# Kernel optimization log

Measured on AMD Instinct MI355X. Metric: run time of the kernel, lower is better.

The kernel has to match this reference:

```python
import jax, jax.numpy as jnp
import numpy as np

B = 1 << 20
N_FREQS = 6          # sin+cos -> 3*2*6 = 36 dims for position
N_BINS = 4           # one-blob bins -> 4 dims per scalar
W_SCALE = 0.18       # ~ sqrt(2/64) He init for ReLU


def freq_embed(p):
    # p: [B,3] -> [B, 3*2*N_FREQS] NeRF-style sin/cos frequency encoding
    freqs = (2.0 ** jnp.arange(N_FREQS, dtype=p.dtype)) * jnp.pi  # [F]
    ang = p[:, :, None] * freqs  # [B,3,F]
    return jnp.concatenate([jnp.sin(ang), jnp.cos(ang)], axis=-1).reshape(p.shape[0], -1)


def one_blob_embed(x):
    # x: [B,D] values in [0,1] -> [B, D*N_BINS] Gaussian one-blob encoding
    centers = (jnp.arange(N_BINS, dtype=x.dtype) + 0.5) / N_BINS  # [K]
    sigma = 1.0 / N_BINS
    val = jnp.exp(-0.5 * ((x[:, :, None] - centers) / sigma) ** 2)  # [B,D,K]
    return val.reshape(x.shape[0], -1)


def to_sphe_coords(d):
    # unit direction [B,3] -> normalized (theta, phi) in [0,1]^2
    theta = jnp.arccos(jnp.clip(d[:, 2], -1.0, 1.0)) / jnp.pi
    phi = jnp.arctan2(d[:, 1], d[:, 0]) / (2.0 * jnp.pi) + 0.5
    return jnp.stack([theta, phi], axis=-1)


def setup_inputs() -> dict:
    key = jax.random.key(0)
    ks = jax.random.split(key, 13)
    p = jax.random.normal(ks[0], (B, 3), dtype=jnp.float32)
    wi = jax.random.normal(ks[1], (B, 3), dtype=jnp.float32)
    wi = wi / jnp.linalg.norm(wi, axis=-1, keepdims=True)
    n = jax.random.normal(ks[2], (B, 3), dtype=jnp.float32)
    n = n / jnp.linalg.norm(n, axis=-1, keepdims=True)
    alpha = jax.random.uniform(ks[3], (B, 3), dtype=jnp.float32)
    beta = jax.random.uniform(ks[4], (B, 3), dtype=jnp.float32)
    r = jax.random.uniform(ks[5], (B, 1), dtype=jnp.float32)
    Ws = {}
    for i in range(6):
        Ws[f"W{i}"] = jax.random.normal(ks[6 + i], (64, 64), dtype=jnp.float32) * W_SCALE
    Ws["W6"] = jax.random.normal(ks[12], (3, 64), dtype=jnp.float32) * W_SCALE
    return dict(p=p, wi=wi, n=n, alpha=alpha, beta=beta, r=r, **Ws)


def reference(p, wi, n, alpha, beta, r, W0, W1, W2, W3, W4, W5, W6):
    x = jnp.concatenate([
        freq_embed(p),                               # 36
        one_blob_embed(to_sphe_coords(wi)),          # 8
        one_blob_embed(to_sphe_coords(n)),           # 8
        one_blob_embed(1.0 - jnp.exp(-r)),           # 4
        alpha,                                       # 3
        beta,                                        # 3
        jnp.ones_like(p[:, :2]),                     # 2 (implicit bias)
    ], axis=-1)  # [B,64]
    h = x
    for W in (W0, W1, W2, W3, W4, W5):
        h = jax.nn.relu(h @ W.T)
    out = h @ W6.T  # [B,3]
    return out * (alpha + beta)  # reflectance factorization
```

## Files before the change

kernel.cpp:

```cpp
#include <hip/hip_runtime.h>

typedef __attribute__((ext_vector_type(8))) short short8;
typedef __attribute__((ext_vector_type(4))) float f32x4;

typedef __attribute__((address_space(3))) unsigned short lds_us;
typedef const __attribute__((address_space(1))) unsigned short glb_us;

__device__ __forceinline__ unsigned short f2bf(float x) {
  union { float f; unsigned u; } v; v.f = x;
  unsigned r = v.u + 0x7fffu + ((v.u >> 16) & 1u);
  return (unsigned short)(r >> 16);
}

#if __has_builtin(__builtin_amdgcn_cvt_pk_bf16_f32)
__device__ __forceinline__ unsigned pk2(float a, float b) {
  return __builtin_bit_cast(unsigned, __builtin_amdgcn_cvt_pk_bf16_f32(a, b));
}
#else
__device__ __forceinline__ unsigned pk2(float a, float b) {
  union { float f; unsigned u; } x, y; x.f = a; y.f = b;
  return __builtin_amdgcn_perm(y.u + 0x8000u, x.u + 0x8000u, 0x07060302u);
}
#endif

__device__ __forceinline__ short8 u2s8(uint4 u) {
  union { uint4 a; short8 b; } c; c.a = u; return c.b;
}

__device__ __forceinline__ void wave_mem_fence() {
  asm volatile("" ::: "memory");
  __builtin_amdgcn_wave_barrier();
  asm volatile("" ::: "memory");
}

__device__ __forceinline__ void gload16(const unsigned short* g, unsigned short* l) {
  __builtin_amdgcn_global_load_lds((glb_us*)g, (lds_us*)l, 16, 0, 0);
}

__device__ __forceinline__ float acos01(float z) {
  float ax = fminf(fabsf(z), 1.0f);
  float t  = __builtin_amdgcn_sqrtf(1.0f - ax);
  float p  = fmaf(ax, fmaf(ax, fmaf(ax, -0.00596110f, 0.02363618f),
                           -0.06751692f), 0.49998766f);
  p *= t;
  return z >= 0.0f ? p : 1.0f - p;
}

__device__ __forceinline__ float atan2_01(float y, float x) {
  float ax = fabsf(x), ay = fabsf(y);
  float hi = fmaxf(ax, ay), lo = fminf(ax, ay);
  float r  = lo * __builtin_amdgcn_rcpf(fmaxf(hi, 1e-30f));
  float r2 = r * r;
  float p  = fmaf(r2, fmaf(r2, fmaf(r2, fmaf(r2, fmaf(r2,
               -0.0018655370f, 0.0083800422f), -0.018531250f),
                0.030803547f), -0.052940457f), 0.159151323f);
  float q  = r * p;
  q = (ay > ax) ? 0.25f - q : q;
  q = (x < 0.0f) ? 0.5f - q : q;
  return 0.5f + ((y >= 0.0f) ? q : -q);
}

__device__ __forceinline__ uint2 blob4pk(float x) {
  float x4 = x * 4.0f;
  float e0, e1, e2, e3;
  { float t = x4 - 0.5f; e0 = __builtin_amdgcn_exp2f(t * t * -0.72134752f); }
  { float t = x4 - 1.5f; e1 = __builtin_amdgcn_exp2f(t * t * -0.72134752f); }
  { float t = x4 - 2.5f; e2 = __builtin_amdgcn_exp2f(t * t * -0.72134752f); }
  { float t = x4 - 3.5f; e3 = __builtin_amdgcn_exp2f(t * t * -0.72134752f); }
  return make_uint2(pk2(e0, e1), pk2(e2, e3));
}

__global__ void prep_weights(
    const float* __restrict__ W0, const float* __restrict__ W1,
    const float* __restrict__ W2, const float* __restrict__ W3,
    const float* __restrict__ W4, const float* __restrict__ W5,
    const float* __restrict__ W6, unsigned short* __restrict__ wb)
{
  int idx = blockIdx.x * blockDim.x + threadIdx.x;
  if (idx < 24576) {
    int l = idx >> 12;
    const float* W = (l==0)?W0:(l==1)?W1:(l==2)?W2:(l==3)?W3:(l==4)?W4:W5;
    int j   = idx & 7;
    int ln  = (idx >> 3) & 63;
    int h   = (idx >> 9) & 1;
    int t   = (idx >> 10) & 3;
    int n15 = ln & 15, q = ln >> 4;
    int src = 32*(t>>1) + 8*(n15>>2) + 4*(t&1) + (n15&3);
    int col = h*32 + q*8 + j;
    wb[idx] = f2bf(W[src*64 + col]);
  } else if (idx < 25600) {
    int i6  = idx - 24576;
    int j   = i6 & 7;
    int ln  = (i6 >> 3) & 63;
    int h   = (i6 >> 9) & 1;
    int n15 = ln & 15, q = ln >> 4;
    wb[idx] = (n15 < 3) ? f2bf(W6[n15*64 + h*32 + q*8 + j]) : (unsigned short)0;
  }
}

__global__ __launch_bounds__(256, 4) void nrc_mlp(
    const float* __restrict__ P, const float* __restrict__ WI,
    const float* __restrict__ NRM, const float* __restrict__ ALPHA,
    const float* __restrict__ BETA, const float* __restrict__ R,
    const unsigned short* __restrict__ wb, float* __restrict__ out)
{
  __shared__ __align__(16) unsigned short lds[20480];
  unsigned short* Wb = lds;
  const int lane = threadIdx.x & 63;
  const int wv   = threadIdx.x >> 6;
  unsigned short* Xw = lds + 4096 + (wv << 12);
  const int n15 = lane & 15;
  const int q   = lane >> 4;
  const int row0 = (blockIdx.x * 4 + wv) * 64;
  const int l16 = lane * 8;

  {
    int c0 = 2*wv*512;
    gload16(wb + c0 + l16,        Wb + c0 + l16);
    gload16(wb + c0 + 512 + l16,  Wb + c0 + 512 + l16);
  }

  {
    const int row = row0 + lane;
    const int sw  = lane & 7;
    unsigned short* xr = Xw + (lane << 6);
#define XST(j) (*(uint4*)(xr + (((j) ^ sw) << 3)))

    float s0[6], c0[6], s1[6], c1[6], s2[6], c2[6];
    {
      float rev = 0.5f * P[row*3+0];
#pragma unroll
      for (int i = 0; i < 6; ++i) {
        float fr = __builtin_amdgcn_fractf(rev);
        s0[i] = __builtin_amdgcn_sinf(fr);
        c0[i] = __builtin_amdgcn_cosf(fr);
        rev = rev + rev;
      }
      rev = 0.5f * P[row*3+1];
#pragma unroll
      for (int i = 0; i < 6; ++i) {
        float fr = __builtin_amdgcn_fractf(rev);
        s1[i] = __builtin_amdgcn_sinf(fr);
        c1[i] = __builtin_amdgcn_cosf(fr);
        rev = rev + rev;
      }
      rev = 0.5f * P[row*3+2];
#pragma unroll
      for (int i = 0; i < 6; ++i) {
        float fr = __builtin_amdgcn_fractf(rev);
        s2[i] = __builtin_amdgcn_sinf(fr);
        c2[i] = __builtin_amdgcn_cosf(fr);
        rev = rev + rev;
      }
    }
    XST(0) = make_uint4(pk2(s0[0],s0[1]), pk2(s0[2],s0[3]),
                        pk2(s0[4],s0[5]), pk2(c0[0],c0[1]));
    XST(1) = make_uint4(pk2(c0[2],c0[3]), pk2(c0[4],c0[5]),
                        pk2(s1[0],s1[1]), pk2(s1[2],s1[3]));
    XST(2) = make_uint4(pk2(s1[4],s1[5]), pk2(c1[0],c1[1]),
                        pk2(c1[2],c1[3]), pk2(c1[4],c1[5]));
    XST(3) = make_uint4(pk2(s2[0],s2[1]), pk2(s2[2],s2[3]),
                        pk2(s2[4],s2[5]), pk2(c2[0],c2[1]));

    uint2 bwt, bwp, bnt, bnp, brr;
    {
      float wx = WI[row*3+0], wy = WI[row*3+1], wz = WI[row*3+2];
      bwt = blob4pk(acos01(wz));
      bwp = blob4pk(atan2_01(wy, wx));
    }
    {
      float nx = NRM[row*3+0], ny = NRM[row*3+1], nz = NRM[row*3+2];
      bnt = blob4pk(acos01(nz));
      bnp = blob4pk(atan2_01(ny, nx));
    }
    brr = blob4pk(1.0f - __builtin_amdgcn_exp2f(R[row] * -1.44269504f));

    XST(4) = make_uint4(pk2(c2[2],c2[3]), pk2(c2[4],c2[5]), bwt.x, bwt.y);
    XST(5) = make_uint4(bwp.x, bwp.y, bnt.x, bnt.y);
    XST(6) = make_uint4(bnp.x, bnp.y, brr.x, brr.y);

    float a0 = ALPHA[row*3+0], a1 = ALPHA[row*3+1], a2 = ALPHA[row*3+2];
    float e0 = BETA[row*3+0],  e1 = BETA[row*3+1],  e2 = BETA[row*3+2];
    XST(7) = make_uint4(pk2(a0,a1), pk2(a2,e0), pk2(e1,e2), 0x3F803F80u);
#undef XST
  }
  wave_mem_fence();

  uint4 b0[4], b1[4];
  {
    const int swr = n15 & 7;
#pragma unroll
    for (int g = 0; g < 4; ++g) {
      const unsigned short* rb = Xw + ((g*16 + n15) << 6);
      b0[g] = *(const uint4*)(rb + (((q    ) ^ swr) << 3));
      b1[g] = *(const uint4*)(rb + (((q + 4) ^ swr) << 3));
    }
  }

  __syncthreads();

  const f32x4 z = {0.f, 0.f, 0.f, 0.f};

#pragma unroll
  for (int l = 0; l < 6; ++l) {
    short8 a0[4], a1[4];
#pragma unroll
    for (int t = 0; t < 4; ++t) {
      a0[t] = *(const short8*)(Wb + t*1024 + l16);
      a1[t] = *(const short8*)(Wb + t*1024 + 512 + l16);
    }
    __syncthreads();

    if (l < 5) {
      int ns = (l+1) * 4096;
      int c0 = 2*wv*512;
      gload16(wb + ns + c0 + l16,       Wb + c0 + l16);
      gload16(wb + ns + c0 + 512 + l16, Wb + c0 + 512 + l16);
    } else if (wv < 2) {
      int c0 = wv*512;
      gload16(wb + 24576 + c0 + l16, Wb + c0 + l16);
    }

#pragma unroll
    for (int g = 0; g < 4; ++g) {
      short8 bb0 = u2s8(b0[g]);
      short8 bb1 = u2s8(b1[g]);
      f32x4 acc[4];
#pragma unroll
      for (int t = 0; t < 4; ++t) {
        f32x4 c = __builtin_amdgcn_mfma_f32_16x16x32_bf16(a0[t], bb0, z, 0, 0, 0);
        acc[t]  = __builtin_amdgcn_mfma_f32_16x16x32_bf16(a1[t], bb1, c, 0, 0, 0);
      }
      uint4 n0, n1;
      n0.x = pk2(fmaxf(acc[0][0],0.f), fmaxf(acc[0][1],0.f));
      n0.y = pk2(fmaxf(acc[0][2],0.f), fmaxf(acc[0][3],0.f));
      n0.z = pk2(fmaxf(acc[1][0],0.f), fmaxf(acc[1][1],0.f));
      n0.w = pk2(fmaxf(acc[1][2],0.f), fmaxf(acc[1][3],0.f));
      n1.x = pk2(fmaxf(acc[2][0],0.f), fmaxf(acc[2][1],0.f));
      n1.y = pk2(fmaxf(acc[2][2],0.f), fmaxf(acc[2][3],0.f));
      n1.z = pk2(fmaxf(acc[3][0],0.f), fmaxf(acc[3][1],0.f));
      n1.w = pk2(fmaxf(acc[3][2],0.f), fmaxf(acc[3][3],0.f));
      b0[g] = n0; b1[g] = n1;
    }
    __syncthreads();
  }

  {
    short8 o0 = *(const short8*)(Wb + l16);
    short8 o1 = *(const short8*)(Wb + 512 + l16);
#pragma unroll
    for (int g = 0; g < 4; ++g) {
      f32x4 c = __builtin_amdgcn_mfma_f32_16x16x32_bf16(o0, u2s8(b0[g]), z, 0, 0, 0);
      c       = __builtin_amdgcn_mfma_f32_16x16x32_bf16(o1, u2s8(b1[g]), c, 0, 0, 0);
      if (q == 0) {
        int base = row0*3 + g*48 + n15*3;
        float3 av = *(const float3*)(ALPHA + base);
        float3 bv = *(const float3*)(BETA + base);
        float3 o;
        o.x = c[0] * (av.x + bv.x);
        o.y = c[1] * (av.y + bv.y);
        o.z = c[2] * (av.z + bv.z);
        *(float3*)(out + base) = o;
      }
    }
  }
}

extern "C" void kernel_launch(void* const* d_in, const int* in_sizes, int n_in,
                              void* d_out, int out_size, void* d_ws, size_t ws_size,
                              hipStream_t stream) {
  const float* P  = (const float*)d_in[0];
  const float* WI = (const float*)d_in[1];
  const float* NR = (const float*)d_in[2];
  const float* AL = (const float*)d_in[3];
  const float* BE = (const float*)d_in[4];
  const float* R  = (const float*)d_in[5];
  const float* W0 = (const float*)d_in[6];
  const float* W1 = (const float*)d_in[7];
  const float* W2 = (const float*)d_in[8];
  const float* W3 = (const float*)d_in[9];
  const float* W4 = (const float*)d_in[10];
  const float* W5 = (const float*)d_in[11];
  const float* W6 = (const float*)d_in[12];
  unsigned short* wb = (unsigned short*)d_ws;
  float* out = (float*)d_out;

  prep_weights<<<100, 256, 0, stream>>>(W0, W1, W2, W3, W4, W5, W6, wb);
  nrc_mlp<<<4096, 256, 0, stream>>>(P, WI, NR, AL, BE, R, wb, out);
}
```

Measured before the change: 175.6 us.

## Use double-angle recurrence, packed bf16 ReLU, and interleaved MFMA issue order

Three separate changes. The frequency encoding now evaluates sin/cos once per coordinate and derives the higher octaves with double-angle recurrences, which replaces hardware transcendentals with multiplies at some cost in accuracy as errors compound. ReLU is applied after packing to bf16 using a packed signed 16-bit max, halving the max instructions. The MFMA loop issues all 16 output tiles before the activation epilogue to give the matrix pipe independent work, using more accumulator registers.

```diff
diff --git a/kernel.cpp b/kernel.cpp
--- a/kernel.cpp
+++ b/kernel.cpp
@@ -22,6 +22,12 @@
   return __builtin_amdgcn_perm(y.u + 0x8000u, x.u + 0x8000u, 0x07060302u);
 }
 #endif
+
+__device__ __forceinline__ unsigned relu_pk(unsigned x) {
+  unsigned r;
+  asm("v_pk_max_i16 %0, %1, %2" : "=v"(r) : "v"(x), "v"(0));
+  return r;
+}
 
 __device__ __forceinline__ short8 u2s8(uint4 u) {
   union { uint4 a; short8 b; } c; c.a = u; return c.b;
@@ -68,6 +74,21 @@
   { float t = x4 - 2.5f; e2 = __builtin_amdgcn_exp2f(t * t * -0.72134752f); }
   { float t = x4 - 3.5f; e3 = __builtin_amdgcn_exp2f(t * t * -0.72134752f); }
   return make_uint2(pk2(e0, e1), pk2(e2, e3));
+}
+
+__device__ __forceinline__ void freq6(float p, float* s, float* c) {
+  float fr = __builtin_amdgcn_fractf(0.5f * p);
+  float sv = __builtin_amdgcn_sinf(fr);
+  float cv = __builtin_amdgcn_cosf(fr);
+  s[0] = sv; c[0] = cv;
+#pragma unroll
+  for (int i = 1; i < 6; ++i) {
+    float t  = sv * cv;
+    float ss = sv * sv;
+    sv = t + t;
+    cv = 1.0f - (ss + ss);
+    s[i] = sv; c[i] = cv;
+  }
 }
 
 __global__ void prep_weights(
@@ -127,32 +148,10 @@
 #define XST(j) (*(uint4*)(xr + (((j) ^ sw) << 3)))
 
     float s0[6], c0[6], s1[6], c1[6], s2[6], c2[6];
-    {
-      float rev = 0.5f * P[row*3+0];
-#pragma unroll
-      for (int i = 0; i < 6; ++i) {
-        float fr = __builtin_amdgcn_fractf(rev);
-        s0[i] = __builtin_amdgcn_sinf(fr);
-        c0[i] = __builtin_amdgcn_cosf(fr);
-        rev = rev + rev;
-      }
-      rev = 0.5f * P[row*3+1];
-#pragma unroll
-      for (int i = 0; i < 6; ++i) {
-        float fr = __builtin_amdgcn_fractf(rev);
-        s1[i] = __builtin_amdgcn_sinf(fr);
-        c1[i] = __builtin_amdgcn_cosf(fr);
-        rev = rev + rev;
-      }
-      rev = 0.5f * P[row*3+2];
-#pragma unroll
-      for (int i = 0; i < 6; ++i) {
-        float fr = __builtin_amdgcn_fractf(rev);
-        s2[i] = __builtin_amdgcn_sinf(fr);
-        c2[i] = __builtin_amdgcn_cosf(fr);
-        rev = rev + rev;
-      }
-    }
+    freq6(P[row*3+0], s0, c0);
+    freq6(P[row*3+1], s1, c1);
+    freq6(P[row*3+2], s2, c2);
+
     XST(0) = make_uint4(pk2(s0[0],s0[1]), pk2(s0[2],s0[3]),
                         pk2(s0[4],s0[5]), pk2(c0[0],c0[1]));
     XST(1) = make_uint4(pk2(c0[2],c0[3]), pk2(c0[4],c0[5]),
@@ -221,25 +220,27 @@
       gload16(wb + 24576 + c0 + l16, Wb + c0 + l16);
     }
 
+    f32x4 acc[4][4];
+#pragma unroll
+    for (int t = 0; t < 4; ++t) {
+#pragma unroll
+      for (int g = 0; g < 4; ++g) {
+        f32x4 c = __builtin_amdgcn_mfma_f32_16x16x32_bf16(a0[t], u2s8(b0[g]), z, 0, 0, 0);
+        acc[g][t] = __builtin_amdgcn_mfma_f32_16x16x32_bf16(a1[t], u2s8(b1[g]), c, 0, 0, 0);
+      }
+    }
+
 #pragma unroll
     for (int g = 0; g < 4; ++g) {
-      short8 bb0 = u2s8(b0[g]);
-      short8 bb1 = u2s8(b1[g]);
-      f32x4 acc[4];
-#pragma unroll
-      for (int t = 0; t < 4; ++t) {
-        f32x4 c = __builtin_amdgcn_mfma_f32_16x16x32_bf16(a0[t], bb0, z, 0, 0, 0);
-        acc[t]  = __builtin_amdgcn_mfma_f32_16x16x32_bf16(a1[t], bb1, c, 0, 0, 0);
-      }
       uint4 n0, n1;
-      n0.x = pk2(fmaxf(acc[0][0],0.f), fmaxf(acc[0][1],0.f));
-      n0.y = pk2(fmaxf(acc[0][2],0.f), fmaxf(acc[0][3],0.f));
-      n0.z = pk2(fmaxf(acc[1][0],0.f), fmaxf(acc[1][1],0.f));
-      n0.w = pk2(fmaxf(acc[1][2],0.f), fmaxf(acc[1][3],0.f));
-      n1.x = pk2(fmaxf(acc[2][0],0.f), fmaxf(acc[2][1],0.f));
-      n1.y = pk2(fmaxf(acc[2][2],0.f), fmaxf(acc[2][3],0.f));
-      n1.z = pk2(fmaxf(acc[3][0],0.f), fmaxf(acc[3][1],0.f));
-      n1.w = pk2(fmaxf(acc[3][2],0.f), fmaxf(acc[3][3],0.f));
+      n0.x = relu_pk(pk2(acc[g][0][0], acc[g][0][1]));
+      n0.y = relu_pk(pk2(acc[g][0][2], acc[g][0][3]));
+      n0.z = relu_pk(pk2(acc[g][1][0], acc[g][1][1]));
+      n0.w = relu_pk(pk2(acc[g][1][2], acc[g][1][3]));
+      n1.x = relu_pk(pk2(acc[g][2][0], acc[g][2][1]));
+      n1.y = relu_pk(pk2(acc[g][2][2], acc[g][2][3]));
+      n1.z = relu_pk(pk2(acc[g][3][0], acc[g][3][1]));
+      n1.w = relu_pk(pk2(acc[g][3][2], acc[g][3][3]));
       b0[g] = n0; b1[g] = n1;
     }
     __syncthreads();
```

Measured after the change: 160.5 us. 1.09x faster.
